# Optimization experiments

Measured on AMD Instinct MI355X. Metric: run time of the kernel, lower is better.

Reference implementation:

```python
import jax, jax.numpy as jnp
import numpy as np

N = 200000      # nodes
C = 256         # scalar channels
VC = 16         # vector channels
VD = 3          # vector spatial dim
M = 50000       # number of motifs (segments)


def setup_inputs() -> dict:
    key = jax.random.key(0)
    ks, kv, kb, kw1, kb1, kw2, kb2 = jax.random.split(key, 7)
    s = jax.random.normal(ks, (N, C), dtype=jnp.float32)
    v = jax.random.normal(kv, (N, VC, VD), dtype=jnp.float32)
    motif_batch = jax.random.randint(kb, (N,), 0, M, dtype=jnp.int64)
    # Linear(channels, channels)
    Ws = jax.random.normal(kw1, (C, C), dtype=jnp.float32) / np.sqrt(C)
    bs = jax.random.normal(kb1, (C,), dtype=jnp.float32) * 0.01
    # Linear(16, 16)
    Wv = jax.random.normal(kw2, (VC, VC), dtype=jnp.float32) / np.sqrt(VC)
    bv = jax.random.normal(kb2, (VC,), dtype=jnp.float32) * 0.01
    return {"s": s, "v": v, "motif_batch": motif_batch,
            "Ws": Ws, "bs": bs, "Wv": Wv, "bv": bv}


def _scatter_mean(x, seg, num_segments):
    # robust scatter mean: sum / max(count, 1)
    sums = jax.ops.segment_sum(x, seg, num_segments=num_segments)
    cnt = jax.ops.segment_sum(jnp.ones((x.shape[0],), x.dtype), seg,
                              num_segments=num_segments)
    cnt = jnp.maximum(cnt, 1.0)
    return sums / cnt.reshape((num_segments,) + (1,) * (x.ndim - 1))


def reference(s, v, motif_batch, Ws, bs, Wv, bv):
    seg = motif_batch.reshape(-1)
    s_motif = _scatter_mean(s, seg, M)            # [M, C]
    v_motif = _scatter_mean(v, seg, M)            # [M, VC, VD]
    s_out = s_motif @ Ws.T + bs                   # [M, C]
    # v_pool(v_motif.transpose(1,2)).transpose(1,2):
    # Linear over the VC axis, spatial dim untouched
    v_out = jnp.einsum('mcd,oc->mod', v_motif, Wv) + bv[None, :, None]
    return (s_out, v_out)
```

## Files before the change

kernel.cpp:

```cpp
#include <hip/hip_runtime.h>

#define N_NODES 200000
#define C 256
#define VC 16
#define VD 3
#define VDIM (VC * VD)
#define M_MOTIFS 50000
#define M_PAD 50048
#define CAP 64

#define NODE_BLOCKS ((N_NODES + 255) / 256)
#define CVT_BLOCKS  ((C * C) / (256 * 4))
#define GATHER_BLOCKS (M_MOTIFS / 4)

typedef __attribute__((ext_vector_type(8))) __bf16 bf16x8;
typedef __attribute__((ext_vector_type(4))) float f32x4;

__device__ __forceinline__ unsigned short f2bf(float x) {
  unsigned u = __builtin_bit_cast(unsigned, x);
  u += 0x7fffu + ((u >> 16) & 1u);
  return (unsigned short)(u >> 16);
}

__device__ __forceinline__ void async_copy16(const void* g, void* l) {
  __builtin_amdgcn_global_load_lds(
      (const __attribute__((address_space(1))) unsigned int*)g,
      (__attribute__((address_space(3))) unsigned int*)l, 16, 0, 0);
}

__global__ __launch_bounds__(256) void fill_kernel(
    const int* __restrict__ seg, int* __restrict__ cnt,
    int* __restrict__ nodelist, const float* __restrict__ Ws,
    unsigned short* __restrict__ Wsb) {
  int b = blockIdx.x, t = threadIdx.x;
  if (b < NODE_BLOCKS) {
    int i = b * 256 + t;
    if (i < N_NODES) {
      int m = seg[i];
      int r = atomicAdd(&cnt[m], 1);
      if (r < CAP) nodelist[(size_t)m * CAP + r] = i;
    }
  } else {
    int i = ((b - NODE_BLOCKS) * 256 + t) * 4;
    float4 w = *(const float4*)(Ws + i);
    ushort4 o;
    o.x = f2bf(w.x); o.y = f2bf(w.y); o.z = f2bf(w.z); o.w = f2bf(w.w);
    *(ushort4*)(Wsb + i) = o;
  }
}

__global__ __launch_bounds__(256) void gather_kernel(
    const float* __restrict__ s, const float* __restrict__ v,
    const int* __restrict__ cnt, const int* __restrict__ nodelist,
    const float* __restrict__ Wv, const float* __restrict__ bv,
    unsigned short* __restrict__ s_motif, float* __restrict__ v_out) {
  int m = (blockIdx.x * 256 + threadIdx.x) >> 6;
  int lane = threadIdx.x & 63;
  int k = cnt[m];

  if (k == 0) {
    ushort4 z; z.x = z.y = z.z = z.w = 0;
    ((ushort4*)(s_motif + (size_t)m * C))[lane] = z;
    if (lane < VDIM) v_out[(size_t)m * VDIM + lane] = bv[lane / 3];
    return;
  }

  int idv = nodelist[(size_t)m * CAP + (lane & 15)];
  int km1 = k - 1;
  int kc = min(k, CAP);

  int i0 = __shfl(idv, 0, 64);
  int i1 = __shfl(idv, min(1, km1), 64);
  int i2 = __shfl(idv, min(2, km1), 64);
  int i3 = __shfl(idv, min(3, km1), 64);
  float4 a0 = ((const float4*)(s + (size_t)i0 * C))[lane];
  float4 a1 = ((const float4*)(s + (size_t)i1 * C))[lane];
  float4 a2 = ((const float4*)(s + (size_t)i2 * C))[lane];
  float4 a3 = ((const float4*)(s + (size_t)i3 * C))[lane];
  float vb0 = 0.f, vb1 = 0.f, vb2 = 0.f, vb3 = 0.f;
  if (lane < VDIM) {
    vb0 = v[(size_t)i0 * VDIM + lane];
    vb1 = v[(size_t)i1 * VDIM + lane];
    vb2 = v[(size_t)i2 * VDIM + lane];
    vb3 = v[(size_t)i3 * VDIM + lane];
  }
  float4 acc = a0;
  float vacc = vb0;
  if (k > 1) { acc.x += a1.x; acc.y += a1.y; acc.z += a1.z; acc.w += a1.w; vacc += vb1; }
  if (k > 2) { acc.x += a2.x; acc.y += a2.y; acc.z += a2.z; acc.w += a2.w; vacc += vb2; }
  if (k > 3) { acc.x += a3.x; acc.y += a3.y; acc.z += a3.z; acc.w += a3.w; vacc += vb3; }

  if (k > 4) {
    int i4 = __shfl(idv, min(4, km1), 64);
    int i5 = __shfl(idv, min(5, km1), 64);
    int i6 = __shfl(idv, min(6, km1), 64);
    int i7 = __shfl(idv, min(7, km1), 64);
    float4 b4 = ((const float4*)(s + (size_t)i4 * C))[lane];
    float4 b5 = ((const float4*)(s + (size_t)i5 * C))[lane];
    float4 b6 = ((const float4*)(s + (size_t)i6 * C))[lane];
    float4 b7 = ((const float4*)(s + (size_t)i7 * C))[lane];
    float w4 = 0.f, w5 = 0.f, w6 = 0.f, w7 = 0.f;
    if (lane < VDIM) {
      w4 = v[(size_t)i4 * VDIM + lane];
      w5 = v[(size_t)i5 * VDIM + lane];
      w6 = v[(size_t)i6 * VDIM + lane];
      w7 = v[(size_t)i7 * VDIM + lane];
    }
    acc.x += b4.x; acc.y += b4.y; acc.z += b4.z; acc.w += b4.w; vacc += w4;
    if (k > 5) { acc.x += b5.x; acc.y += b5.y; acc.z += b5.z; acc.w += b5.w; vacc += w5; }
    if (k > 6) { acc.x += b6.x; acc.y += b6.y; acc.z += b6.z; acc.w += b6.w; vacc += w6; }
    if (k > 7) { acc.x += b7.x; acc.y += b7.y; acc.z += b7.z; acc.w += b7.w; vacc += w7; }
  }

  if (k > 8) {
    int idv2 = nodelist[(size_t)m * CAP + lane];
    for (int j = 8; j < kc; ++j) {
      int ij = __shfl(idv2, j, 64);
      float4 a = ((const float4*)(s + (size_t)ij * C))[lane];
      acc.x += a.x; acc.y += a.y; acc.z += a.z; acc.w += a.w;
      if (lane < VDIM) vacc += v[(size_t)ij * VDIM + lane];
    }
  }

  float rc = 1.0f / (float)k;
  ushort4 o;
  o.x = f2bf(acc.x * rc); o.y = f2bf(acc.y * rc);
  o.z = f2bf(acc.z * rc); o.w = f2bf(acc.w * rc);
  ((ushort4*)(s_motif + (size_t)m * C))[lane] = o;

  float vm = vacc * rc;
  if (lane < VDIM) {
    int oo = lane / 3, d = lane - oo * 3;
    float vo = bv[oo];
#pragma unroll
    for (int c2 = 0; c2 < VC; ++c2)
      vo += Wv[oo * VC + c2] * __shfl(vm, c2 * 3 + d, 64);
    v_out[(size_t)m * VDIM + lane] = vo;
  }
}

__global__ __launch_bounds__(256) void gemm_mfma_kernel(
    const unsigned short* __restrict__ A16,
    const unsigned short* __restrict__ B16,
    const float* __restrict__ bs, float* __restrict__ out) {
  __shared__ unsigned short As[128 * 32];
  __shared__ unsigned short Bs[128 * 32];
  int tid = threadIdx.x;
  int wave = tid >> 6, lane = tid & 63;
  int m0 = blockIdx.x * 128;
  int n0 = blockIdx.y * 128;
  int wm = (wave >> 1) * 64, wn = (wave & 1) * 64;

  f32x4 acc[4][4] = {};

  int srow = lane >> 2;
  int kc   = (lane & 3) * 8;
  int rl = lane & 15;
  int kq = (lane >> 4) * 8;

  const unsigned short* Ag = A16 + (size_t)(m0 + wave * 32) * C;
  const unsigned short* Bg = B16 + (size_t)(n0 + wave * 32) * C;
  unsigned short* Al = As + wave * 32 * 32;
  unsigned short* Bl = Bs + wave * 32 * 32;

  for (int k0 = 0; k0 < C; k0 += 32) {
    async_copy16(Ag + (size_t)srow * C + k0 + kc, Al);
    async_copy16(Ag + (size_t)(16 + srow) * C + k0 + kc, Al + 16 * 32);
    async_copy16(Bg + (size_t)srow * C + k0 + kc, Bl);
    async_copy16(Bg + (size_t)(16 + srow) * C + k0 + kc, Bl + 16 * 32);
    __syncthreads();

    bf16x8 af[4], bfr[4];
#pragma unroll
    for (int i = 0; i < 4; ++i)
      af[i] = *(const bf16x8*)&As[(size_t)(wm + i * 16 + rl) * 32 + kq];
#pragma unroll
    for (int j = 0; j < 4; ++j)
      bfr[j] = *(const bf16x8*)&Bs[(size_t)(wn + j * 16 + rl) * 32 + kq];
#pragma unroll
    for (int i = 0; i < 4; ++i)
#pragma unroll
      for (int j = 0; j < 4; ++j)
        acc[i][j] = __builtin_amdgcn_mfma_f32_16x16x32_bf16(
            af[i], bfr[j], acc[i][j], 0, 0, 0);
    __syncthreads();
  }

  int rq = (lane >> 4) * 4;
#pragma unroll
  for (int j = 0; j < 4; ++j) {
    int cn = n0 + wn + j * 16 + rl;
    float bias = bs[cn];
#pragma unroll
    for (int i = 0; i < 4; ++i) {
#pragma unroll
      for (int r = 0; r < 4; ++r) {
        int gm = m0 + wm + i * 16 + rq + r;
        if (gm < M_MOTIFS) out[(size_t)gm * C + cn] = acc[i][j][r] + bias;
      }
    }
  }
}

extern "C" void kernel_launch(void* const* d_in, const int* in_sizes, int n_in,
                              void* d_out, int out_size, void* d_ws, size_t ws_size,
                              hipStream_t stream) {
  const float* s  = (const float*)d_in[0];
  const float* v  = (const float*)d_in[1];
  const int*   seg = (const int*)d_in[2];
  const float* Ws = (const float*)d_in[3];
  const float* bs = (const float*)d_in[4];
  const float* Wv = (const float*)d_in[5];
  const float* bv = (const float*)d_in[6];

  float* out   = (float*)d_out;
  float* s_out = out;
  float* v_out = out + (size_t)M_MOTIFS * C;

  int* cnt      = (int*)d_ws;
  int* nodelist = cnt + M_MOTIFS;
  unsigned short* Wsb     = (unsigned short*)(nodelist + (size_t)M_MOTIFS * CAP);
  unsigned short* s_motif = Wsb + (size_t)C * C;

  hipMemsetAsync(cnt, 0, M_MOTIFS * sizeof(int), stream);
  fill_kernel<<<NODE_BLOCKS + CVT_BLOCKS, 256, 0, stream>>>(seg, cnt, nodelist,
                                                            Ws, Wsb);
  gather_kernel<<<GATHER_BLOCKS, 256, 0, stream>>>(s, v, cnt, nodelist, Wv, bv,
                                                   s_motif, v_out);
  {
    dim3 grid(M_PAD / 128, C / 128);
    gemm_mfma_kernel<<<grid, 256, 0, stream>>>(s_motif, Wsb, bs, s_out);
  }
}
```

Measured before the change: 104.1 us.

## Load GEMM operands directly from global memory and issue all eight gather loads eagerly

```diff
diff --git a/kernel.cpp b/kernel.cpp
--- a/kernel.cpp
+++ b/kernel.cpp
@@ -12,6 +12,7 @@
 #define NODE_BLOCKS ((N_NODES + 255) / 256)
 #define CVT_BLOCKS  ((C * C) / (256 * 4))
 #define GATHER_BLOCKS (M_MOTIFS / 4)
+#define GEMM_BLOCKS (M_PAD / 64)
 
 typedef __attribute__((ext_vector_type(8))) __bf16 bf16x8;
 typedef __attribute__((ext_vector_type(4))) float f32x4;
@@ -20,12 +21,6 @@
   unsigned u = __builtin_bit_cast(unsigned, x);
   u += 0x7fffu + ((u >> 16) & 1u);
   return (unsigned short)(u >> 16);
-}
-
-__device__ __forceinline__ void async_copy16(const void* g, void* l) {
-  __builtin_amdgcn_global_load_lds(
-      (const __attribute__((address_space(1))) unsigned int*)g,
-      (__attribute__((address_space(3))) unsigned int*)l, 16, 0, 0);
 }
 
 __global__ __launch_bounds__(256) void fill_kernel(
@@ -56,7 +51,9 @@
     unsigned short* __restrict__ s_motif, float* __restrict__ v_out) {
   int m = (blockIdx.x * 256 + threadIdx.x) >> 6;
   int lane = threadIdx.x & 63;
+
   int k = cnt[m];
+  int idv = nodelist[(size_t)m * CAP + (lane & 15)];
 
   if (k == 0) {
     ushort4 z; z.x = z.y = z.z = z.w = 0;
@@ -65,7 +62,6 @@
     return;
   }
 
-  int idv = nodelist[(size_t)m * CAP + (lane & 15)];
   int km1 = k - 1;
   int kc = min(k, CAP);
 
@@ -73,44 +69,39 @@
   int i1 = __shfl(idv, min(1, km1), 64);
   int i2 = __shfl(idv, min(2, km1), 64);
   int i3 = __shfl(idv, min(3, km1), 64);
+  int i4 = __shfl(idv, min(4, km1), 64);
+  int i5 = __shfl(idv, min(5, km1), 64);
+  int i6 = __shfl(idv, min(6, km1), 64);
+  int i7 = __shfl(idv, min(7, km1), 64);
   float4 a0 = ((const float4*)(s + (size_t)i0 * C))[lane];
   float4 a1 = ((const float4*)(s + (size_t)i1 * C))[lane];
   float4 a2 = ((const float4*)(s + (size_t)i2 * C))[lane];
   float4 a3 = ((const float4*)(s + (size_t)i3 * C))[lane];
+  float4 a4 = ((const float4*)(s + (size_t)i4 * C))[lane];
+  float4 a5 = ((const float4*)(s + (size_t)i5 * C))[lane];
+  float4 a6 = ((const float4*)(s + (size_t)i6 * C))[lane];
+  float4 a7 = ((const float4*)(s + (size_t)i7 * C))[lane];
   float vb0 = 0.f, vb1 = 0.f, vb2 = 0.f, vb3 = 0.f;
+  float vb4 = 0.f, vb5 = 0.f, vb6 = 0.f, vb7 = 0.f;
   if (lane < VDIM) {
     vb0 = v[(size_t)i0 * VDIM + lane];
     vb1 = v[(size_t)i1 * VDIM + lane];
     vb2 = v[(size_t)i2 * VDIM + lane];
     vb3 = v[(size_t)i3 * VDIM + lane];
+    vb4 = v[(size_t)i4 * VDIM + lane];
+    vb5 = v[(size_t)i5 * VDIM + lane];
+    vb6 = v[(size_t)i6 * VDIM + lane];
+    vb7 = v[(size_t)i7 * VDIM + lane];
   }
   float4 acc = a0;
   float vacc = vb0;
   if (k > 1) { acc.x += a1.x; acc.y += a1.y; acc.z += a1.z; acc.w += a1.w; vacc += vb1; }
   if (k > 2) { acc.x += a2.x; acc.y += a2.y; acc.z += a2.z; acc.w += a2.w; vacc += vb2; }
   if (k > 3) { acc.x += a3.x; acc.y += a3.y; acc.z += a3.z; acc.w += a3.w; vacc += vb3; }
-
-  if (k > 4) {
-    int i4 = __shfl(idv, min(4, km1), 64);
-    int i5 = __shfl(idv, min(5, km1), 64);
-    int i6 = __shfl(idv, min(6, km1), 64);
-    int i7 = __shfl(idv, min(7, km1), 64);
-    float4 b4 = ((const float4*)(s + (size_t)i4 * C))[lane];
-    float4 b5 = ((const float4*)(s + (size_t)i5 * C))[lane];
-    float4 b6 = ((const float4*)(s + (size_t)i6 * C))[lane];
-    float4 b7 = ((const float4*)(s + (size_t)i7 * C))[lane];
-    float w4 = 0.f, w5 = 0.f, w6 = 0.f, w7 = 0.f;
-    if (lane < VDIM) {
-      w4 = v[(size_t)i4 * VDIM + lane];
-      w5 = v[(size_t)i5 * VDIM + lane];
-      w6 = v[(size_t)i6 * VDIM + lane];
-      w7 = v[(size_t)i7 * VDIM + lane];
-    }
-    acc.x += b4.x; acc.y += b4.y; acc.z += b4.z; acc.w += b4.w; vacc += w4;
-    if (k > 5) { acc.x += b5.x; acc.y += b5.y; acc.z += b5.z; acc.w += b5.w; vacc += w5; }
-    if (k > 6) { acc.x += b6.x; acc.y += b6.y; acc.z += b6.z; acc.w += b6.w; vacc += w6; }
-    if (k > 7) { acc.x += b7.x; acc.y += b7.y; acc.z += b7.z; acc.w += b7.w; vacc += w7; }
-  }
+  if (k > 4) { acc.x += a4.x; acc.y += a4.y; acc.z += a4.z; acc.w += a4.w; vacc += vb4; }
+  if (k > 5) { acc.x += a5.x; acc.y += a5.y; acc.z += a5.z; acc.w += a5.w; vacc += vb5; }
+  if (k > 6) { acc.x += a6.x; acc.y += a6.y; acc.z += a6.z; acc.w += a6.w; vacc += vb6; }
+  if (k > 7) { acc.x += a7.x; acc.y += a7.y; acc.z += a7.z; acc.w += a7.w; vacc += vb7; }
 
   if (k > 8) {
     int idv2 = nodelist[(size_t)m * CAP + lane];
@@ -139,63 +130,47 @@
   }
 }
 
-__global__ __launch_bounds__(256) void gemm_mfma_kernel(
+__global__ __launch_bounds__(256) void gemm_direct_kernel(
     const unsigned short* __restrict__ A16,
     const unsigned short* __restrict__ B16,
     const float* __restrict__ bs, float* __restrict__ out) {
-  __shared__ unsigned short As[128 * 32];
-  __shared__ unsigned short Bs[128 * 32];
   int tid = threadIdx.x;
   int wave = tid >> 6, lane = tid & 63;
-  int m0 = blockIdx.x * 128;
-  int n0 = blockIdx.y * 128;
-  int wm = (wave >> 1) * 64, wn = (wave & 1) * 64;
+  int m0 = blockIdx.x * 64;
+  int wn0 = wave * 64;
+  int rl = lane & 15, kq = (lane >> 4) * 8;
+
+  const unsigned short* Ab = A16 + (size_t)(m0 + rl) * C + kq;
+  const unsigned short* Bb = B16 + (size_t)(wn0 + rl) * C + kq;
 
   f32x4 acc[4][4] = {};
-
-  int srow = lane >> 2;
-  int kc   = (lane & 3) * 8;
-  int rl = lane & 15;
-  int kq = (lane >> 4) * 8;
-
-  const unsigned short* Ag = A16 + (size_t)(m0 + wave * 32) * C;
-  const unsigned short* Bg = B16 + (size_t)(n0 + wave * 32) * C;
-  unsigned short* Al = As + wave * 32 * 32;
-  unsigned short* Bl = Bs + wave * 32 * 32;
-
+#pragma unroll 2
   for (int k0 = 0; k0 < C; k0 += 32) {
-    async_copy16(Ag + (size_t)srow * C + k0 + kc, Al);
-    async_copy16(Ag + (size_t)(16 + srow) * C + k0 + kc, Al + 16 * 32);
-    async_copy16(Bg + (size_t)srow * C + k0 + kc, Bl);
-    async_copy16(Bg + (size_t)(16 + srow) * C + k0 + kc, Bl + 16 * 32);
-    __syncthreads();
-
     bf16x8 af[4], bfr[4];
 #pragma unroll
     for (int i = 0; i < 4; ++i)
-      af[i] = *(const bf16x8*)&As[(size_t)(wm + i * 16 + rl) * 32 + kq];
+      af[i] = *(const bf16x8*)(Ab + (size_t)i * 16 * C + k0);
 #pragma unroll
     for (int j = 0; j < 4; ++j)
-      bfr[j] = *(const bf16x8*)&Bs[(size_t)(wn + j * 16 + rl) * 32 + kq];
+      bfr[j] = *(const bf16x8*)(Bb + (size_t)j * 16 * C + k0);
 #pragma unroll
     for (int i = 0; i < 4; ++i)
 #pragma unroll
       for (int j = 0; j < 4; ++j)
         acc[i][j] = __builtin_amdgcn_mfma_f32_16x16x32_bf16(
             af[i], bfr[j], acc[i][j], 0, 0, 0);
-    __syncthreads();
   }
 
   int rq = (lane >> 4) * 4;
 #pragma unroll
   for (int j = 0; j < 4; ++j) {
-    int cn = n0 + wn + j * 16 + rl;
+    int cn = wn0 + j * 16 + rl;
     float bias = bs[cn];
 #pragma unroll
     for (int i = 0; i < 4; ++i) {
 #pragma unroll
       for (int r = 0; r < 4; ++r) {
-        int gm = m0 + wm + i * 16 + rq + r;
+        int gm = m0 + i * 16 + rq + r;
         if (gm < M_MOTIFS) out[(size_t)gm * C + cn] = acc[i][j][r] + bias;
       }
     }
@@ -227,8 +202,5 @@
                                                             Ws, Wsb);
   gather_kernel<<<GATHER_BLOCKS, 256, 0, stream>>>(s, v, cnt, nodelist, Wv, bv,
                                                    s_motif, v_out);
-  {
-    dim3 grid(M_PAD / 128, C / 128);
-    gemm_mfma_kernel<<<grid, 256, 0, stream>>>(s_motif, Wsb, bs, s_out);
-  }
-}
+  gemm_direct_kernel<<<GEMM_BLOCKS, 256, 0, stream>>>(s_motif, Wsb, bs, s_out);
+}
```

Result: slower. 129.3 us (+24.2%).

## Use persistent GEMM with half of Ws resident in swizzled LDS

Applied to the files above, without the earlier changes.

```diff
diff --git a/kernel.cpp b/kernel.cpp
--- a/kernel.cpp
+++ b/kernel.cpp
@@ -12,6 +12,8 @@
 #define NODE_BLOCKS ((N_NODES + 255) / 256)
 #define CVT_BLOCKS  ((C * C) / (256 * 4))
 #define GATHER_BLOCKS (M_MOTIFS / 4)
+#define GEMM_BLOCKS 512
+#define NTILES (M_PAD / 64)
 
 typedef __attribute__((ext_vector_type(8))) __bf16 bf16x8;
 typedef __attribute__((ext_vector_type(4))) float f32x4;
@@ -20,12 +22,6 @@
   unsigned u = __builtin_bit_cast(unsigned, x);
   u += 0x7fffu + ((u >> 16) & 1u);
   return (unsigned short)(u >> 16);
-}
-
-__device__ __forceinline__ void async_copy16(const void* g, void* l) {
-  __builtin_amdgcn_global_load_lds(
-      (const __attribute__((address_space(1))) unsigned int*)g,
-      (__attribute__((address_space(3))) unsigned int*)l, 16, 0, 0);
 }
 
 __global__ __launch_bounds__(256) void fill_kernel(
@@ -56,7 +52,9 @@
     unsigned short* __restrict__ s_motif, float* __restrict__ v_out) {
   int m = (blockIdx.x * 256 + threadIdx.x) >> 6;
   int lane = threadIdx.x & 63;
+
   int k = cnt[m];
+  int idv = nodelist[(size_t)m * CAP + (lane & 15)];
 
   if (k == 0) {
     ushort4 z; z.x = z.y = z.z = z.w = 0;
@@ -65,7 +63,6 @@
     return;
   }
 
-  int idv = nodelist[(size_t)m * CAP + (lane & 15)];
   int km1 = k - 1;
   int kc = min(k, CAP);
 
@@ -139,64 +136,65 @@
   }
 }
 
-__global__ __launch_bounds__(256) void gemm_mfma_kernel(
+__global__ __launch_bounds__(256, 2) void gemm_persistB_kernel(
     const unsigned short* __restrict__ A16,
     const unsigned short* __restrict__ B16,
     const float* __restrict__ bs, float* __restrict__ out) {
-  __shared__ unsigned short As[128 * 32];
-  __shared__ unsigned short Bs[128 * 32];
+  __shared__ unsigned short Bs[128 * 256];
   int tid = threadIdx.x;
+  int half = blockIdx.x & 1;
+  int bstart = blockIdx.x >> 1;
+  int n0 = half * 128;
+
+#pragma unroll
+  for (int it = 0; it < 16; ++it) {
+    int chunk = it * 256 + tid;
+    int row = chunk >> 5, cpos = chunk & 31;
+    bf16x8 w = *(const bf16x8*)(B16 + (size_t)(n0 + row) * C + cpos * 8);
+    int byte = row * 512 + ((cpos * 16) ^ ((row & 7) << 4));
+    *(bf16x8*)((char*)Bs + byte) = w;
+  }
+  __syncthreads();
+
   int wave = tid >> 6, lane = tid & 63;
-  int m0 = blockIdx.x * 128;
-  int n0 = blockIdx.y * 128;
-  int wm = (wave >> 1) * 64, wn = (wave & 1) * 64;
-
-  f32x4 acc[4][4] = {};
-
-  int srow = lane >> 2;
-  int kc   = (lane & 3) * 8;
   int rl = lane & 15;
-  int kq = (lane >> 4) * 8;
-
-  const unsigned short* Ag = A16 + (size_t)(m0 + wave * 32) * C;
-  const unsigned short* Bg = B16 + (size_t)(n0 + wave * 32) * C;
-  unsigned short* Al = As + wave * 32 * 32;
-  unsigned short* Bl = Bs + wave * 32 * 32;
-
-  for (int k0 = 0; k0 < C; k0 += 32) {
-    async_copy16(Ag + (size_t)srow * C + k0 + kc, Al);
-    async_copy16(Ag + (size_t)(16 + srow) * C + k0 + kc, Al + 16 * 32);
-    async_copy16(Bg + (size_t)srow * C + k0 + kc, Bl);
-    async_copy16(Bg + (size_t)(16 + srow) * C + k0 + kc, Bl + 16 * 32);
-    __syncthreads();
-
-    bf16x8 af[4], bfr[4];
-#pragma unroll
-    for (int i = 0; i < 4; ++i)
-      af[i] = *(const bf16x8*)&As[(size_t)(wm + i * 16 + rl) * 32 + kq];
-#pragma unroll
-    for (int j = 0; j < 4; ++j)
-      bfr[j] = *(const bf16x8*)&Bs[(size_t)(wn + j * 16 + rl) * 32 + kq];
-#pragma unroll
-    for (int i = 0; i < 4; ++i)
-#pragma unroll
-      for (int j = 0; j < 4; ++j)
-        acc[i][j] = __builtin_amdgcn_mfma_f32_16x16x32_bf16(
-            af[i], bfr[j], acc[i][j], 0, 0, 0);
-    __syncthreads();
-  }
-
-  int rq = (lane >> 4) * 4;
-#pragma unroll
-  for (int j = 0; j < 4; ++j) {
-    int cn = n0 + wn + j * 16 + rl;
-    float bias = bs[cn];
-#pragma unroll
-    for (int i = 0; i < 4; ++i) {
+  int quad = lane >> 4;
+  int kq = quad * 8;
+  int rq = quad * 4;
+
+  float bias[8];
+#pragma unroll
+  for (int j = 0; j < 8; ++j) bias[j] = bs[n0 + j * 16 + rl];
+
+  for (int t = bstart; t < NTILES; t += 256) {
+    int m0 = t * 64;
+    int mrow = m0 + wave * 16 + rl;
+    const unsigned short* Ab = A16 + (size_t)mrow * C + kq;
+    bf16x8 af[8];
+#pragma unroll
+    for (int kk = 0; kk < 8; ++kk)
+      af[kk] = *(const bf16x8*)(Ab + kk * 32);
+
+    f32x4 acc[8] = {};
+#pragma unroll
+    for (int kk = 0; kk < 8; ++kk) {
+#pragma unroll
+      for (int j = 0; j < 8; ++j) {
+        int rowl = j * 16 + rl;
+        int byte = rowl * 512 + ((kk * 64 + quad * 16) ^ ((rowl & 7) << 4));
+        bf16x8 bf = *(const bf16x8*)((const char*)Bs + byte);
+        acc[j] = __builtin_amdgcn_mfma_f32_16x16x32_bf16(af[kk], bf, acc[j],
+                                                         0, 0, 0);
+      }
+    }
+
+#pragma unroll
+    for (int j = 0; j < 8; ++j) {
+      int cn = n0 + j * 16 + rl;
 #pragma unroll
       for (int r = 0; r < 4; ++r) {
-        int gm = m0 + wm + i * 16 + rq + r;
-        if (gm < M_MOTIFS) out[(size_t)gm * C + cn] = acc[i][j][r] + bias;
+        int gm = m0 + wave * 16 + rq + r;
+        if (gm < M_MOTIFS) out[(size_t)gm * C + cn] = acc[j][r] + bias[j];
       }
     }
   }
@@ -227,8 +225,5 @@
                                                             Ws, Wsb);
   gather_kernel<<<GATHER_BLOCKS, 256, 0, stream>>>(s, v, cnt, nodelist, Wv, bv,
                                                    s_motif, v_out);
-  {
-    dim3 grid(M_PAD / 128, C / 128);
-    gemm_mfma_kernel<<<grid, 256, 0, stream>>>(s_motif, Wsb, bs, s_out);
-  }
-}
+  gemm_persistB_kernel<<<GEMM_BLOCKS, 256, 0, stream>>>(s_motif, Wsb, bs, s_out);
+}
```

New measurement: 127.7 us. 22.7% more time.
